# Kernel tuning notes

Hardware: AMD Instinct MI355X
Metric: run time of the kernel (lower is better)

The kernel has to match this reference:

```python
import jax, jax.numpy as jnp
import numpy as np

B, D, R = 8192, 4096, 64
REG_W, REG_C = 0.01, 0.05


def setup_inputs() -> dict:
    key = jax.random.key(0)
    ks = jax.random.split(key, 7)
    return {
        "X": jax.random.normal(ks[0], (B, D), dtype=jnp.float32),
        "U1": jax.random.normal(ks[1], (1, D, R), dtype=jnp.float32),
        "U2": jax.random.normal(ks[2], (2, D, R), dtype=jnp.float32),
        "U3": jax.random.normal(ks[3], (3, D, R), dtype=jnp.float32),
        "C": jax.random.normal(ks[4], (3,), dtype=jnp.float32),
        "beta": jax.random.normal(ks[5], (1,), dtype=jnp.float32),
        "C_sin": jax.random.normal(ks[6], (1,), dtype=jnp.float32),
    }


def reference(X, U1, U2, U3, C, beta, C_sin):
    # term_j(x) = sum_r prod_{i<=j} <x, U_j[i, :, r]>
    result = jnp.broadcast_to(beta[0], (X.shape[0],))
    reg_loss_w = jnp.float32(0.0)
    for j, U in enumerate((U1, U2, U3)):
        dots = jnp.einsum("bd,odr->obr", X, U)      # [order, B, R]
        term = jnp.prod(dots, axis=0).sum(axis=1)   # [B]
        result = result + C[j] * term
        reg_loss_w = reg_loss_w + REG_W * (jnp.abs(U).sum() / U.size)
    sine_term = C_sin[0] * jnp.sin(X).sum(axis=1)
    result = result + sine_term
    reg_loss_c = REG_C * (jnp.abs(C).sum() + jnp.abs(C_sin).sum())
    total_reg = reg_loss_w + reg_loss_c
    return result, total_reg
```

## Files before the change

### kernel.cpp

```cpp
#include <hip/hip_runtime.h>
#include <hip/hip_bf16.h>

typedef float f32x4 __attribute__((ext_vector_type(4)));
typedef short s16x8 __attribute__((ext_vector_type(8)));

#define D_DIM 4096
#define NT 24
#define BM 128
#define KS 4
#define NBODY 16
#define SINW_OFF 3145728u
#define PART_OFF 3276800u
#define SWZ(a) ((a) ^ ((((a) >> 7) & 7) << 4))

__device__ __forceinline__ unsigned short f2bf(float f) {
    unsigned u = __float_as_uint(f);
    u += 0x7fffu + ((u >> 16) & 1u);
    return (unsigned short)(u >> 16);
}

__global__ __launch_bounds__(64) void reg_init_kernel(const float* __restrict__ C,
                                                      const float* __restrict__ Csin,
                                                      float* __restrict__ reg_out) {
    if (threadIdx.x == 0)
        reg_out[0] = 0.05f * (fabsf(C[0]) + fabsf(C[1]) + fabsf(C[2]) + fabsf(Csin[0]));
}

__global__ __launch_bounds__(64) void build_w_kernel(const float* __restrict__ U1,
                                                     const float* __restrict__ U2,
                                                     const float* __restrict__ U3,
                                                     unsigned short* __restrict__ W,
                                                     float* __restrict__ reg_out) {
    const int ks = blockIdx.x / NT;
    const int ct = blockIdx.x % NT;
    const int l  = threadIdx.x;
    const int n  = ct * 16 + (l & 15);
    const int kb = ks * 32 + ((l >> 4) << 3);

    const float* src;
    float scale;
    if (n < 64)       { src = U1 + n;                  scale = 0.01f / 262144.f; }
    else if (n < 128) { src = U2 + (n - 64);           scale = 0.01f / 524288.f; }
    else if (n < 192) { src = U2 + 262144 + (n - 128); scale = 0.01f / 524288.f; }
    else if (n < 256) { src = U3 + (n - 192);          scale = 0.01f / 786432.f; }
    else if (n < 320) { src = U3 + 262144 + (n - 256); scale = 0.01f / 786432.f; }
    else              { src = U3 + 524288 + (n - 320); scale = 0.01f / 786432.f; }

    unsigned short h[8];
    float sabs = 0.f;
#pragma unroll
    for (int j = 0; j < 8; ++j) {
        float u = src[(size_t)(kb + j) * 64];
        sabs += fabsf(u);
        h[j] = f2bf(u);
    }
    uint4 pk;
    pk.x = (unsigned)h[0] | ((unsigned)h[1] << 16);
    pk.y = (unsigned)h[2] | ((unsigned)h[3] << 16);
    pk.z = (unsigned)h[4] | ((unsigned)h[5] << 16);
    pk.w = (unsigned)h[6] | ((unsigned)h[7] << 16);
    *(uint4*)(W + ((size_t)blockIdx.x * 64 + l) * 8) = pk;

    sabs *= scale;
#pragma unroll
    for (int off = 32; off >= 1; off >>= 1)
        sabs += __shfl_xor(sabs, off, 64);
    if (l == 0) atomicAdd(reg_out, sabs);
}

__global__ __launch_bounds__(512, 2) void poly_main_kernel(const float* __restrict__ X,
                                                           const unsigned short* __restrict__ W,
                                                           _Float16* __restrict__ part,
                                                           float* __restrict__ sinws) {
    __shared__ __align__(16) char pool[32768];

    const int t    = threadIdx.x;
    const int lane = t & 63;
    const int wv   = t >> 6;
    const int rg   = wv >> 2;
    const int cg   = wv & 3;
    const int ct0  = cg * 6;
    const int rb   = blockIdx.x >> 2;
    const int ks   = blockIdx.x & 3;
    const int row0 = rb * BM;

    const int srow = t >> 2;
    const int k16  = (t & 3) << 4;
    const float* xp = X + (size_t)(row0 + srow) * D_DIM + ks * 1024 + k16;
    const int kslot_s = k16 >> 5;
    const int ch0     = (k16 & 31) >> 3;
    const int fragw   = kslot_s * 8 + (srow >> 4);
    const int aw0 = SWZ(fragw * 1024 + (((ch0 + 0) << 4) | (srow & 15)) * 16);
    const int aw1 = SWZ(fragw * 1024 + (((ch0 + 1) << 4) | (srow & 15)) * 16);

    const s16x8* __restrict__ Wf = (const s16x8*)W;

    f32x4 acc[4][6];
#pragma unroll
    for (int r = 0; r < 4; ++r)
#pragma unroll
        for (int c = 0; c < 6; ++c) acc[r][c] = (f32x4){0.f, 0.f, 0.f, 0.f};
    float sinacc = 0.f;

    f32x4 xA0, xA1, xA2, xA3, xB0, xB1, xB2, xB3;

#define LOADX(S0, S1, S2, S3, slab)                                             \
    { const float* _p = xp + (size_t)(slab) * 64;                               \
      S0 = *(const f32x4*)(_p);      S1 = *(const f32x4*)(_p + 4);              \
      S2 = *(const f32x4*)(_p + 8);  S3 = *(const f32x4*)(_p + 12); }

#define STAGE(buf, S0, S1, S2, S3)                                              \
    {                                                                           \
        sinacc += __sinf(S0.x) + __sinf(S0.y) + __sinf(S0.z) + __sinf(S0.w)     \
                + __sinf(S1.x) + __sinf(S1.y) + __sinf(S1.z) + __sinf(S1.w)     \
                + __sinf(S2.x) + __sinf(S2.y) + __sinf(S2.z) + __sinf(S2.w)     \
                + __sinf(S3.x) + __sinf(S3.y) + __sinf(S3.z) + __sinf(S3.w);    \
        uint4 lo, hi;                                                           \
        lo.x = (unsigned)f2bf(S0.x) | ((unsigned)f2bf(S0.y) << 16);             \
        lo.y = (unsigned)f2bf(S0.z) | ((unsigned)f2bf(S0.w) << 16);             \
        lo.z = (unsigned)f2bf(S1.x) | ((unsigned)f2bf(S1.y) << 16);             \
        lo.w = (unsigned)f2bf(S1.z) | ((unsigned)f2bf(S1.w) << 16);             \
        hi.x = (unsigned)f2bf(S2.x) | ((unsigned)f2bf(S2.y) << 16);             \
        hi.y = (unsigned)f2bf(S2.z) | ((unsigned)f2bf(S2.w) << 16);             \
        hi.z = (unsigned)f2bf(S3.x) | ((unsigned)f2bf(S3.y) << 16);             \
        hi.w = (unsigned)f2bf(S3.z) | ((unsigned)f2bf(S3.w) << 16);             \
        *(uint4*)(pool + (buf) * 16384 + aw0) = lo;                             \
        *(uint4*)(pool + (buf) * 16384 + aw1) = hi;                             \
    }

    LOADX(xA0, xA1, xA2, xA3, 0);
    STAGE(0, xA0, xA1, xA2, xA3);
    LOADX(xB0, xB1, xB2, xB3, 1);
    asm volatile("s_waitcnt lgkmcnt(0)" ::: "memory");
    __builtin_amdgcn_s_barrier();
    __builtin_amdgcn_sched_barrier(0);

#define BODY(d_, XS0, XS1, XS2, XS3, XL0, XL1, XL2, XL3)                        \
    {                                                                           \
        const int d__ = (d_);                                                   \
        const int sb_ = ks * 32 + 2 * d__;                                      \
        s16x8 bb[2][6];                                                         \
        _Pragma("unroll")                                                       \
        for (int kk = 0; kk < 2; ++kk)                                          \
            _Pragma("unroll")                                                   \
            for (int c = 0; c < 6; ++c)                                         \
                bb[kk][c] = Wf[((size_t)(sb_ + kk) * NT + ct0 + c) * 64 + lane];\
        int sl_ = d__ + 2; if (sl_ > NBODY - 1) sl_ = NBODY - 1;                \
        LOADX(XL0, XL1, XL2, XL3, sl_);                                         \
        if (d__ < NBODY - 1) { STAGE((d__ + 1) & 1, XS0, XS1, XS2, XS3); }      \
        const int ab_ = (d__ & 1) * 16384;                                      \
        s16x8 af[2][4];                                                         \
        _Pragma("unroll")                                                       \
        for (int kk = 0; kk < 2; ++kk)                                          \
            _Pragma("unroll")                                                   \
            for (int rf = 0; rf < 4; ++rf)                                      \
                af[kk][rf] = *(const s16x8*)(pool + ab_ +                       \
                    SWZ((kk * 8 + rg * 4 + rf) * 1024 + lane * 16));            \
        asm volatile("s_waitcnt lgkmcnt(0)" ::: "memory");                      \
        __builtin_amdgcn_sched_barrier(0);                                      \
        __builtin_amdgcn_s_setprio(1);                                          \
        _Pragma("unroll")                                                       \
        for (int kk = 0; kk < 2; ++kk)                                          \
            _Pragma("unroll")                                                   \
            for (int rf = 0; rf < 4; ++rf)                                      \
                _Pragma("unroll")                                               \
                for (int c = 0; c < 6; ++c)                                     \
                    acc[rf][c] = __builtin_amdgcn_mfma_f32_16x16x32_bf16(       \
                        af[kk][rf], bb[kk][c], acc[rf][c], 0, 0, 0);            \
        __builtin_amdgcn_s_setprio(0);                                          \
        __builtin_amdgcn_s_barrier();                                           \
        __builtin_amdgcn_sched_barrier(0);                                      \
    }

    for (int e = 0; e < 8; ++e) {
        BODY(2 * e,     xB0, xB1, xB2, xB3, xA0, xA1, xA2, xA3);
        BODY(2 * e + 1, xA0, xA1, xA2, xA3, xB0, xB1, xB2, xB3);
    }
#undef BODY
#undef STAGE
#undef LOADX

    _Float16* pb = part + (size_t)ks * 8192 * 384;
    const int lr4 = (lane >> 4) << 2;
    const int lc  = lane & 15;
#pragma unroll
    for (int rf = 0; rf < 4; ++rf)
#pragma unroll
        for (int c = 0; c < 6; ++c) {
            const int col = (ct0 + c) * 16 + lc;
#pragma unroll
            for (int i = 0; i < 4; ++i) {
                const int rl = rg * 64 + rf * 16 + lr4 + i;
                pb[(size_t)(row0 + rl) * 384 + col] = (_Float16)acc[rf][c][i];
            }
        }

    sinacc += __shfl_xor(sinacc, 1);
    sinacc += __shfl_xor(sinacc, 2);
    if ((t & 3) == 0)
        sinws[(size_t)ks * 8192 + row0 + srow] = sinacc;
}

__global__ __launch_bounds__(512) void combine_kernel(const _Float16* __restrict__ part,
                                                      const float* __restrict__ sinws,
                                                      const float* __restrict__ C,
                                                      const float* __restrict__ beta,
                                                      const float* __restrict__ Csin,
                                                      float* __restrict__ out) {
    const int t   = threadIdx.x;
    const int row = blockIdx.x * 32 + (t >> 4);
    const int cc  = t & 15;
    const size_t rbase = (size_t)row * 384;

    float t1 = 0.f, t2 = 0.f, t3 = 0.f;
#pragma unroll
    for (int j = 0; j < 4; ++j) {
        const int c = j * 16 + cc;
        float a1 = 0.f, a2 = 0.f, b2 = 0.f, a3 = 0.f, b3 = 0.f, c3 = 0.f;
#pragma unroll
        for (int q = 0; q < 4; ++q) {
            const _Float16* p = part + (size_t)q * 8192 * 384 + rbase;
            a1 += (float)p[c];
            a2 += (float)p[64 + c];
            b2 += (float)p[128 + c];
            a3 += (float)p[192 + c];
            b3 += (float)p[256 + c];
            c3 += (float)p[320 + c];
        }
        t1 += a1;
        t2 += a2 * b2;
        t3 += a3 * b3 * c3;
    }
#pragma unroll
    for (int off = 1; off < 16; off <<= 1) {
        t1 += __shfl_xor(t1, off, 16);
        t2 += __shfl_xor(t2, off, 16);
        t3 += __shfl_xor(t3, off, 16);
    }
    if (cc == 0) {
        const float s = sinws[row] + sinws[8192 + row]
                      + sinws[2 * 8192 + row] + sinws[3 * 8192 + row];
        out[row] = beta[0] + C[0] * t1 + C[1] * t2 + C[2] * t3 + Csin[0] * s;
    }
}

extern "C" void kernel_launch(void* const* d_in, const int* in_sizes, int n_in,
                              void* d_out, int out_size, void* d_ws, size_t ws_size,
                              hipStream_t stream) {
    const float* X   = (const float*)d_in[0];
    const float* U1  = (const float*)d_in[1];
    const float* U2  = (const float*)d_in[2];
    const float* U3  = (const float*)d_in[3];
    const float* Cc  = (const float*)d_in[4];
    const float* bet = (const float*)d_in[5];
    const float* Cs  = (const float*)d_in[6];
    float* out = (float*)d_out;

    unsigned short* W = (unsigned short*)d_ws;
    float* sinws = (float*)((char*)d_ws + SINW_OFF);
    _Float16* part = (_Float16*)((char*)d_ws + PART_OFF);

    reg_init_kernel<<<1, 64, 0, stream>>>(Cc, Cs, out + 8192);
    build_w_kernel<<<128 * NT, 64, 0, stream>>>(U1, U2, U3, W, out + 8192);
    poly_main_kernel<<<256, 512, 0, stream>>>(X, W, part, sinws);
    combine_kernel<<<256, 512, 0, stream>>>(part, sinws, Cc, bet, Cs, out);
}
```

Before: 96.51 us.

## Stage W tiles into LDS via global_load_lds with 1024-thread blocks

The main GEMM kernel now runs 16 waves per block, each computing a 64x48 tile, and processes the K-slice in 32 steps of 32 instead of 16 steps of 64. W fragments are no longer loaded straight into registers from global memory; they are copied asynchronously into a double-buffered LDS region with global_load_lds, and each wave reads its B fragments from LDS. X staging is spread over more threads with smaller per-thread loads. The aim is more in-flight memory traffic and lower register pressure per wave, at the cost of twice as many barriers, more LDS use (64KB), and removal of the LDS swizzle, which may cause bank conflicts.

After: 98.03 us. No clear change (+1.6%).

```diff
diff --git a/kernel.cpp b/kernel.cpp
--- a/kernel.cpp
+++ b/kernel.cpp
@@ -7,16 +7,22 @@
 #define D_DIM 4096
 #define NT 24
 #define BM 128
-#define KS 4
-#define NBODY 16
+#define NBODY 32
+#define BOFF 0
+#define AOFF 49152
 #define SINW_OFF 3145728u
 #define PART_OFF 3276800u
-#define SWZ(a) ((a) ^ ((((a) >> 7) & 7) << 4))
 
 __device__ __forceinline__ unsigned short f2bf(float f) {
     unsigned u = __float_as_uint(f);
     u += 0x7fffu + ((u >> 16) & 1u);
     return (unsigned short)(u >> 16);
+}
+
+__device__ __forceinline__ void gload16(const void* g, void* l) {
+    __builtin_amdgcn_global_load_lds(
+        (const __attribute__((address_space(1))) unsigned int*)g,
+        (__attribute__((address_space(3))) unsigned int*)l, 16, 0, 0);
 }
 
 __global__ __launch_bounds__(64) void reg_init_kernel(const float* __restrict__ C,
@@ -68,137 +74,134 @@
     if (l == 0) atomicAdd(reg_out, sabs);
 }
 
-__global__ __launch_bounds__(512, 2) void poly_main_kernel(const float* __restrict__ X,
-                                                           const unsigned short* __restrict__ W,
-                                                           _Float16* __restrict__ part,
-                                                           float* __restrict__ sinws) {
-    __shared__ __align__(16) char pool[32768];
+__global__ __launch_bounds__(1024, 4) void poly_main_kernel(const float* __restrict__ X,
+                                                            const unsigned short* __restrict__ W,
+                                                            _Float16* __restrict__ part,
+                                                            float* __restrict__ sinws) {
+    __shared__ __align__(16) char pool[65536];
 
     const int t    = threadIdx.x;
     const int lane = t & 63;
     const int wv   = t >> 6;
-    const int rg   = wv >> 2;
-    const int cg   = wv & 3;
-    const int ct0  = cg * 6;
+    const int rg   = wv >> 3;
+    const int cg   = wv & 7;
+    const int ct0  = cg * 3;
     const int rb   = blockIdx.x >> 2;
     const int ks   = blockIdx.x & 3;
     const int row0 = rb * BM;
 
-    const int srow = t >> 2;
-    const int k16  = (t & 3) << 4;
-    const float* xp = X + (size_t)(row0 + srow) * D_DIM + ks * 1024 + k16;
-    const int kslot_s = k16 >> 5;
-    const int ch0     = (k16 & 31) >> 3;
-    const int fragw   = kslot_s * 8 + (srow >> 4);
-    const int aw0 = SWZ(fragw * 1024 + (((ch0 + 0) << 4) | (srow & 15)) * 16);
-    const int aw1 = SWZ(fragw * 1024 + (((ch0 + 1) << 4) | (srow & 15)) * 16);
-
-    const s16x8* __restrict__ Wf = (const s16x8*)W;
-
-    f32x4 acc[4][6];
-#pragma unroll
-    for (int r = 0; r < 4; ++r)
-#pragma unroll
-        for (int c = 0; c < 6; ++c) acc[r][c] = (f32x4){0.f, 0.f, 0.f, 0.f};
+    const int sr = t >> 3;
+    const int k4 = (t & 7) << 2;
+    const float* xp = X + (size_t)(row0 + sr) * D_DIM + ks * 1024 + k4;
+    const int awfrag = (sr >> 4) * 1024
+                     + ((((k4 >> 3) << 4) | (sr & 15)) * 16) + ((k4 & 7) << 1);
+
+    const int nB  = (wv < 8) ? 2 : 1;
+    const int ch0 = (wv < 8) ? (wv * 2) : (wv + 8);
+    const int slab0 = ks * 32;
+
+    f32x4 acc00{}, acc01{}, acc02{}, acc10{}, acc11{}, acc12{},
+          acc20{}, acc21{}, acc22{}, acc30{}, acc31{}, acc32{};
     float sinacc = 0.f;
 
-    f32x4 xA0, xA1, xA2, xA3, xB0, xB1, xB2, xB3;
-
-#define LOADX(S0, S1, S2, S3, slab)                                             \
-    { const float* _p = xp + (size_t)(slab) * 64;                               \
-      S0 = *(const f32x4*)(_p);      S1 = *(const f32x4*)(_p + 4);              \
-      S2 = *(const f32x4*)(_p + 8);  S3 = *(const f32x4*)(_p + 12); }
-
-#define STAGE(buf, S0, S1, S2, S3)                                              \
+#define STAGE(bufl, XV)                                                         \
     {                                                                           \
-        sinacc += __sinf(S0.x) + __sinf(S0.y) + __sinf(S0.z) + __sinf(S0.w)     \
-                + __sinf(S1.x) + __sinf(S1.y) + __sinf(S1.z) + __sinf(S1.w)     \
-                + __sinf(S2.x) + __sinf(S2.y) + __sinf(S2.z) + __sinf(S2.w)     \
-                + __sinf(S3.x) + __sinf(S3.y) + __sinf(S3.z) + __sinf(S3.w);    \
-        uint4 lo, hi;                                                           \
-        lo.x = (unsigned)f2bf(S0.x) | ((unsigned)f2bf(S0.y) << 16);             \
-        lo.y = (unsigned)f2bf(S0.z) | ((unsigned)f2bf(S0.w) << 16);             \
-        lo.z = (unsigned)f2bf(S1.x) | ((unsigned)f2bf(S1.y) << 16);             \
-        lo.w = (unsigned)f2bf(S1.z) | ((unsigned)f2bf(S1.w) << 16);             \
-        hi.x = (unsigned)f2bf(S2.x) | ((unsigned)f2bf(S2.y) << 16);             \
-        hi.y = (unsigned)f2bf(S2.z) | ((unsigned)f2bf(S2.w) << 16);             \
-        hi.z = (unsigned)f2bf(S3.x) | ((unsigned)f2bf(S3.y) << 16);             \
-        hi.w = (unsigned)f2bf(S3.z) | ((unsigned)f2bf(S3.w) << 16);             \
-        *(uint4*)(pool + (buf) * 16384 + aw0) = lo;                             \
-        *(uint4*)(pool + (buf) * 16384 + aw1) = hi;                             \
-    }
-
-    LOADX(xA0, xA1, xA2, xA3, 0);
-    STAGE(0, xA0, xA1, xA2, xA3);
-    LOADX(xB0, xB1, xB2, xB3, 1);
+        sinacc += __sinf(XV.x) + __sinf(XV.y) + __sinf(XV.z) + __sinf(XV.w);    \
+        uint2 h_;                                                               \
+        h_.x = (unsigned)f2bf(XV.x) | ((unsigned)f2bf(XV.y) << 16);             \
+        h_.y = (unsigned)f2bf(XV.z) | ((unsigned)f2bf(XV.w) << 16);             \
+        *(uint2*)(pool + AOFF + (bufl) * 8192 + awfrag) = h_;                   \
+    }
+
+    {
+        const unsigned short* g0 = W + (size_t)slab0 * 12288 + ch0 * 512 + lane * 8;
+        gload16(g0, pool + BOFF + ch0 * 1024);
+        if (nB == 2) gload16(g0 + 512, pool + BOFF + (ch0 + 1) * 1024);
+    }
+    f32x4 xn;
+    {
+        f32x4 x0 = *(const f32x4*)xp;
+        STAGE(0, x0);
+        xn = *(const f32x4*)(xp + 32);
+    }
     asm volatile("s_waitcnt lgkmcnt(0)" ::: "memory");
+    asm volatile("s_waitcnt vmcnt(1)" ::: "memory");
     __builtin_amdgcn_s_barrier();
     __builtin_amdgcn_sched_barrier(0);
 
-#define BODY(d_, XS0, XS1, XS2, XS3, XL0, XL1, XL2, XL3)                        \
+#define BODY(d_, CUR, NXT)                                                      \
     {                                                                           \
         const int d__ = (d_);                                                   \
-        const int sb_ = ks * 32 + 2 * d__;                                      \
-        s16x8 bb[2][6];                                                         \
-        _Pragma("unroll")                                                       \
-        for (int kk = 0; kk < 2; ++kk)                                          \
-            _Pragma("unroll")                                                   \
-            for (int c = 0; c < 6; ++c)                                         \
-                bb[kk][c] = Wf[((size_t)(sb_ + kk) * NT + ct0 + c) * 64 + lane];\
+        if (d__ + 1 < NBODY) {                                                  \
+            const unsigned short* g_ = W + (size_t)(slab0 + d__ + 1) * 12288    \
+                                         + ch0 * 512 + lane * 8;                \
+            gload16(g_, pool + BOFF + (NXT) * 24576 + ch0 * 1024);              \
+            if (nB == 2)                                                        \
+                gload16(g_ + 512, pool + BOFF + (NXT) * 24576 + (ch0 + 1) * 1024);\
+        }                                                                       \
         int sl_ = d__ + 2; if (sl_ > NBODY - 1) sl_ = NBODY - 1;                \
-        LOADX(XL0, XL1, XL2, XL3, sl_);                                         \
-        if (d__ < NBODY - 1) { STAGE((d__ + 1) & 1, XS0, XS1, XS2, XS3); }      \
-        const int ab_ = (d__ & 1) * 16384;                                      \
-        s16x8 af[2][4];                                                         \
-        _Pragma("unroll")                                                       \
-        for (int kk = 0; kk < 2; ++kk)                                          \
-            _Pragma("unroll")                                                   \
-            for (int rf = 0; rf < 4; ++rf)                                      \
-                af[kk][rf] = *(const s16x8*)(pool + ab_ +                       \
-                    SWZ((kk * 8 + rg * 4 + rf) * 1024 + lane * 16));            \
+        f32x4 xf_ = *(const f32x4*)(xp + (size_t)sl_ * 32);                     \
+        if (d__ + 1 < NBODY) { STAGE(NXT, xn); }                                \
+        xn = xf_;                                                               \
+        const char* ab_ = pool + AOFF + (CUR) * 8192;                           \
+        const char* bb_ = pool + BOFF + (CUR) * 24576;                          \
+        s16x8 af0_ = *(const s16x8*)(ab_ + (rg * 4 + 0) * 1024 + lane * 16);    \
+        s16x8 af1_ = *(const s16x8*)(ab_ + (rg * 4 + 1) * 1024 + lane * 16);    \
+        s16x8 af2_ = *(const s16x8*)(ab_ + (rg * 4 + 2) * 1024 + lane * 16);    \
+        s16x8 af3_ = *(const s16x8*)(ab_ + (rg * 4 + 3) * 1024 + lane * 16);    \
+        s16x8 bf0_ = *(const s16x8*)(bb_ + (ct0 + 0) * 1024 + lane * 16);       \
+        s16x8 bf1_ = *(const s16x8*)(bb_ + (ct0 + 1) * 1024 + lane * 16);       \
+        s16x8 bf2_ = *(const s16x8*)(bb_ + (ct0 + 2) * 1024 + lane * 16);       \
         asm volatile("s_waitcnt lgkmcnt(0)" ::: "memory");                      \
         __builtin_amdgcn_sched_barrier(0);                                      \
         __builtin_amdgcn_s_setprio(1);                                          \
-        _Pragma("unroll")                                                       \
-        for (int kk = 0; kk < 2; ++kk)                                          \
-            _Pragma("unroll")                                                   \
-            for (int rf = 0; rf < 4; ++rf)                                      \
-                _Pragma("unroll")                                               \
-                for (int c = 0; c < 6; ++c)                                     \
-                    acc[rf][c] = __builtin_amdgcn_mfma_f32_16x16x32_bf16(       \
-                        af[kk][rf], bb[kk][c], acc[rf][c], 0, 0, 0);            \
+        acc00 = __builtin_amdgcn_mfma_f32_16x16x32_bf16(af0_, bf0_, acc00, 0, 0, 0); \
+        acc01 = __builtin_amdgcn_mfma_f32_16x16x32_bf16(af0_, bf1_, acc01, 0, 0, 0); \
+        acc02 = __builtin_amdgcn_mfma_f32_16x16x32_bf16(af0_, bf2_, acc02, 0, 0, 0); \
+        acc10 = __builtin_amdgcn_mfma_f32_16x16x32_bf16(af1_, bf0_, acc10, 0, 0, 0); \
+        acc11 = __builtin_amdgcn_mfma_f32_16x16x32_bf16(af1_, bf1_, acc11, 0, 0, 0); \
+        acc12 = __builtin_amdgcn_mfma_f32_16x16x32_bf16(af1_, bf2_, acc12, 0, 0, 0); \
+        acc20 = __builtin_amdgcn_mfma_f32_16x16x32_bf16(af2_, bf0_, acc20, 0, 0, 0); \
+        acc21 = __builtin_amdgcn_mfma_f32_16x16x32_bf16(af2_, bf1_, acc21, 0, 0, 0); \
+        acc22 = __builtin_amdgcn_mfma_f32_16x16x32_bf16(af2_, bf2_, acc22, 0, 0, 0); \
+        acc30 = __builtin_amdgcn_mfma_f32_16x16x32_bf16(af3_, bf0_, acc30, 0, 0, 0); \
+        acc31 = __builtin_amdgcn_mfma_f32_16x16x32_bf16(af3_, bf1_, acc31, 0, 0, 0); \
+        acc32 = __builtin_amdgcn_mfma_f32_16x16x32_bf16(af3_, bf2_, acc32, 0, 0, 0); \
         __builtin_amdgcn_s_setprio(0);                                          \
+        asm volatile("s_waitcnt vmcnt(1)" ::: "memory");                        \
         __builtin_amdgcn_s_barrier();                                           \
         __builtin_amdgcn_sched_barrier(0);                                      \
     }
 
-    for (int e = 0; e < 8; ++e) {
-        BODY(2 * e,     xB0, xB1, xB2, xB3, xA0, xA1, xA2, xA3);
-        BODY(2 * e + 1, xA0, xA1, xA2, xA3, xB0, xB1, xB2, xB3);
+    for (int d = 0; d < NBODY; d += 2) {
+        BODY(d, 0, 1);
+        BODY(d + 1, 1, 0);
     }
 #undef BODY
 #undef STAGE
-#undef LOADX
 
     _Float16* pb = part + (size_t)ks * 8192 * 384;
     const int lr4 = (lane >> 4) << 2;
     const int lc  = lane & 15;
+    const f32x4 accA[4][3] = {{acc00, acc01, acc02}, {acc10, acc11, acc12},
+                              {acc20, acc21, acc22}, {acc30, acc31, acc32}};
 #pragma unroll
     for (int rf = 0; rf < 4; ++rf)
 #pragma unroll
-        for (int c = 0; c < 6; ++c) {
+        for (int c = 0; c < 3; ++c) {
             const int col = (ct0 + c) * 16 + lc;
 #pragma unroll
             for (int i = 0; i < 4; ++i) {
                 const int rl = rg * 64 + rf * 16 + lr4 + i;
-                pb[(size_t)(row0 + rl) * 384 + col] = (_Float16)acc[rf][c][i];
+                pb[(size_t)(row0 + rl) * 384 + col] = (_Float16)accA[rf][c][i];
             }
         }
 
     sinacc += __shfl_xor(sinacc, 1);
     sinacc += __shfl_xor(sinacc, 2);
-    if ((t & 3) == 0)
-        sinws[(size_t)ks * 8192 + row0 + srow] = sinacc;
+    sinacc += __shfl_xor(sinacc, 4);
+    if ((t & 7) == 0)
+        sinws[(size_t)ks * 8192 + row0 + sr] = sinacc;
 }
 
 __global__ __launch_bounds__(512) void combine_kernel(const _Float16* __restrict__ part,
@@ -262,6 +265,6 @@
 
     reg_init_kernel<<<1, 64, 0, stream>>>(Cc, Cs, out + 8192);
     build_w_kernel<<<128 * NT, 64, 0, stream>>>(U1, U2, U3, W, out + 8192);
-    poly_main_kernel<<<256, 512, 0, stream>>>(X, W, part, sinws);
+    poly_main_kernel<<<256, 1024, 0, stream>>>(X, W, part, sinws);
     combine_kernel<<<256, 512, 0, stream>>>(part, sinws, Cc, bet, Cs, out);
 }
```
